# Optimization experiments

Measured on AMD Instinct MI355X. Metric: run time of the kernel, lower is better.

The kernel has to match this reference:

```python
import jax, jax.numpy as jnp
import numpy as np

B, N_HM, K_APP, S = 16, 32, 16, 256

def setup_inputs() -> dict:
    key = jax.random.key(0)
    k1, k2, k3 = jax.random.split(key, 3)
    # x: post-UNet appearance feature map [B, K, S, S]
    x = jax.random.normal(k1, (B, K_APP, S, S), dtype=jnp.float32)
    # raw_tps: raw heatmap logits [B, N, S, S]
    raw_tps = jax.random.normal(k2, (B, N_HM, S, S), dtype=jnp.float32)
    # fitted_cj: non-negative fitted heatmaps [B, N, S, S]
    fitted_cj = jax.random.uniform(k3, (B, N_HM, S, S), dtype=jnp.float32)
    return {"x": x, "raw_tps": raw_tps, "fitted_cj": fitted_cj}

def reference(x, raw_tps, fitted_cj):
    # torch F.softmax on a 2D [S,S] tensor with no dim defaults to dim=1 -> per-row softmax
    p = jax.nn.softmax(raw_tps, axis=-1)                      # [B, N, S, S]
    # attention pooling: app_vec[b,n,k] = sum_{h,w} x[b,k,h,w] * p[b,n,h,w]
    app_vec = jnp.einsum('bkhw,bnhw->bnk', x, p)              # [B, N, K]
    # weighted combine without materializing the [B,N,S,S,K] repeat
    num = jnp.einsum('bnhw,bnk->bhwk', fitted_cj, app_vec)    # [B, S, S, K]
    denom = 1.0 + jnp.sum(fitted_cj, axis=1)[..., None]       # [B, S, S, 1]
    app_enco = num / denom                                     # [B, S, S, K]
    # transpose(2,3) then transpose(1,2): [B,S,S,K] -> [B,K,S,S]
    return jnp.transpose(app_enco, (0, 3, 1, 2))
```

## Files before the change

kernel.cpp:

```cpp
#include <hip/hip_runtime.h>

#define S_DIM 256
#define N_HM 32
#define K_APP 16
#define HG 4

typedef _Float16 half4_t __attribute__((ext_vector_type(4)));
typedef _Float16 half8_t __attribute__((ext_vector_type(8)));
typedef float f32x4 __attribute__((ext_vector_type(4)));

__global__ __launch_bounds__(256, 4) void k1_softmax_pool(
    const float* __restrict__ x,
    const float* __restrict__ raw,
    float* __restrict__ partial)
{
    __shared__ _Float16 p_h[N_HM][264];
    __shared__ _Float16 x_h[K_APP][264];
    __shared__ float    inv_s[N_HM];
    __shared__ float    red[2][64][4];

    const int tid  = threadIdx.x;
    const int wid  = tid >> 6;
    const int lane = tid & 63;
    const int b    = blockIdx.x >> 6;
    const int hg   = blockIdx.x & 63;
    const int h0   = hg * HG;

    const int nh  = wid >> 1;
    const int wq  = wid & 1;
    const int row = lane & 15;
    const int q   = lane >> 4;

    float4 r_raw[8];
    float4 r_x[4];
    f32x4  acc = {0.f, 0.f, 0.f, 0.f};

    {
        const float* rp = raw + (((size_t)(b * N_HM + wid * 8)) << 16) + (h0 << 8) + (lane << 2);
        #pragma unroll
        for (int i = 0; i < 8; ++i) r_raw[i] = *(const float4*)(rp + ((size_t)i << 16));
        const float* xp = x + (((size_t)(b * K_APP + wid * 4)) << 16) + (h0 << 8) + (lane << 2);
        #pragma unroll
        for (int i = 0; i < 4; ++i) r_x[i] = *(const float4*)(xp + ((size_t)i << 16));
    }

    for (int it = 0; it < HG; ++it) {
        #pragma unroll
        for (int i = 0; i < 4; ++i) {
            half4_t hv = { (_Float16)r_x[i].x, (_Float16)r_x[i].y,
                           (_Float16)r_x[i].z, (_Float16)r_x[i].w };
            *(half4_t*)&x_h[wid * 4 + i][lane << 2] = hv;
        }
        #pragma unroll
        for (int i = 0; i < 8; ++i) {
            const int n = wid * 8 + i;
            float e0 = __expf(r_raw[i].x), e1 = __expf(r_raw[i].y);
            float e2 = __expf(r_raw[i].z), e3 = __expf(r_raw[i].w);
            float s = (e0 + e1) + (e2 + e3);
            #pragma unroll
            for (int off = 32; off > 0; off >>= 1) s += __shfl_xor(s, off);
            if (lane == 0) inv_s[n] = 1.0f / s;
            half4_t hv = { (_Float16)e0, (_Float16)e1, (_Float16)e2, (_Float16)e3 };
            *(half4_t*)&p_h[n][lane << 2] = hv;
        }
        __syncthreads();

        if (it + 1 < HG) {
            const int h = h0 + it + 1;
            const float* rp = raw + (((size_t)(b * N_HM + wid * 8)) << 16) + (h << 8) + (lane << 2);
            #pragma unroll
            for (int i = 0; i < 8; ++i) r_raw[i] = *(const float4*)(rp + ((size_t)i << 16));
            const float* xp = x + (((size_t)(b * K_APP + wid * 4)) << 16) + (h << 8) + (lane << 2);
            #pragma unroll
            for (int i = 0; i < 4; ++i) r_x[i] = *(const float4*)(xp + ((size_t)i << 16));
        }

        f32x4 part = {0.f, 0.f, 0.f, 0.f};
        #pragma unroll
        for (int s4 = 0; s4 < 4; ++s4) {
            const int w = wq * 128 + s4 * 32 + q * 8;
            half8_t a = *(const half8_t*)&p_h[nh * 16 + row][w];
            half8_t bb = *(const half8_t*)&x_h[row][w];
            part = __builtin_amdgcn_mfma_f32_16x16x32_f16(a, bb, part, 0, 0, 0);
        }
        const int rb = nh * 16 + q * 4;
        acc.x += part.x * inv_s[rb + 0];
        acc.y += part.y * inv_s[rb + 1];
        acc.z += part.z * inv_s[rb + 2];
        acc.w += part.w * inv_s[rb + 3];
        __syncthreads();
    }

    if (wq == 1) {
        red[nh][lane][0] = acc.x; red[nh][lane][1] = acc.y;
        red[nh][lane][2] = acc.z; red[nh][lane][3] = acc.w;
    }
    __syncthreads();
    if (wq == 0) {
        float* dst = partial + ((size_t)blockIdx.x << 9)
                   + (size_t)(nh * 16 + q * 4) * 16 + row;
        dst[0]  = acc.x + red[nh][lane][0];
        dst[16] = acc.y + red[nh][lane][1];
        dst[32] = acc.z + red[nh][lane][2];
        dst[48] = acc.w + red[nh][lane][3];
    }
}

__global__ __launch_bounds__(256) void k1_reduce(
    const float* __restrict__ partial, float* __restrict__ av)
{
    const int gid = blockIdx.x * 256 + threadIdx.x;
    const int b = gid >> 9;
    const int r = gid & 511;
    const float* p = partial + ((size_t)b << 15) + r;
    float s = 0.0f;
    #pragma unroll 8
    for (int j = 0; j < 64; ++j) s += p[(size_t)j << 9];
    av[gid] = s;
}

__global__ __launch_bounds__(256) void k2_combine(
    const float* __restrict__ fit,
    const float* __restrict__ av,
    float* __restrict__ out)
{
    const int tid = threadIdx.x;
    const int b   = blockIdx.x >> 6;
    const int p4  = ((blockIdx.x & 63) << 8) + tid;

    const float* fb  = fit + (((size_t)(b * N_HM)) << 16) + ((size_t)p4 << 2);
    const float* avb = av + (b << 9);

    float4 num[K_APP];
    #pragma unroll
    for (int k = 0; k < K_APP; ++k) num[k] = make_float4(0.f, 0.f, 0.f, 0.f);
    float4 den = make_float4(1.f, 1.f, 1.f, 1.f);

    #pragma unroll 4
    for (int n = 0; n < N_HM; ++n) {
        float4 f = *(const float4*)(fb + ((size_t)n << 16));
        den.x += f.x; den.y += f.y; den.z += f.z; den.w += f.w;
        const float* a = avb + (n << 4);
        #pragma unroll
        for (int k = 0; k < K_APP; ++k) {
            const float ak = a[k];
            num[k].x += f.x * ak; num[k].y += f.y * ak;
            num[k].z += f.z * ak; num[k].w += f.w * ak;
        }
    }

    const float4 inv = make_float4(1.f / den.x, 1.f / den.y, 1.f / den.z, 1.f / den.w);
    float* ob = out + (((size_t)(b * K_APP)) << 16) + ((size_t)p4 << 2);
    #pragma unroll
    for (int k = 0; k < K_APP; ++k) {
        float4 v = make_float4(num[k].x * inv.x, num[k].y * inv.y,
                               num[k].z * inv.z, num[k].w * inv.w);
        *(float4*)(ob + ((size_t)k << 16)) = v;
    }
}

extern "C" void kernel_launch(void* const* d_in, const int* in_sizes, int n_in,
                              void* d_out, int out_size, void* d_ws, size_t ws_size,
                              hipStream_t stream)
{
    const float* x   = (const float*)d_in[0];
    const float* raw = (const float*)d_in[1];
    const float* fit = (const float*)d_in[2];
    float* out = (float*)d_out;

    float* av      = (float*)d_ws;
    float* partial = (float*)d_ws + 8192;

    k1_softmax_pool<<<16 * (S_DIM / HG), 256, 0, stream>>>(x, raw, partial);
    k1_reduce<<<8192 / 256, 256, 0, stream>>>(partial, av);
    k2_combine<<<16 * 64, 256, 0, stream>>>(fit, av, out);
}
```

Before: 353.1 us.

## Feed MFMA directly from registers, one wave per row and heatmap half

The softmax-pool kernel drops the shared-memory staging, the block barriers and the cross-wave reduction. Each wave now handles one (batch, row, 16-heatmap half): it loads raw and x straight into the MFMA operand layout, computes exp and the row sum in registers, and writes normalized per-row partials. The cost is a partial buffer four times larger and a reduce kernel that sums 256 rows instead of 64. The combine kernel's unroll factor is also raised from 4 to 8.

```diff
diff --git a/kernel.cpp b/kernel.cpp
--- a/kernel.cpp
+++ b/kernel.cpp
@@ -3,107 +3,59 @@
 #define S_DIM 256
 #define N_HM 32
 #define K_APP 16
-#define HG 4
 
-typedef _Float16 half4_t __attribute__((ext_vector_type(4)));
 typedef _Float16 half8_t __attribute__((ext_vector_type(8)));
 typedef float f32x4 __attribute__((ext_vector_type(4)));
 
-__global__ __launch_bounds__(256, 4) void k1_softmax_pool(
+__global__ __launch_bounds__(256) void k1_softmax_pool(
     const float* __restrict__ x,
     const float* __restrict__ raw,
     float* __restrict__ partial)
 {
-    __shared__ _Float16 p_h[N_HM][264];
-    __shared__ _Float16 x_h[K_APP][264];
-    __shared__ float    inv_s[N_HM];
-    __shared__ float    red[2][64][4];
+    const int wid  = threadIdx.x >> 6;
+    const int lane = threadIdx.x & 63;
+    const int gw   = blockIdx.x * 4 + wid;
+    const int pair = gw >> 1;
+    const int nh   = gw & 1;
+    const int b    = pair >> 8;
+    const int h    = pair & 255;
+    const int col  = lane & 15;
+    const int q    = lane >> 4;
 
-    const int tid  = threadIdx.x;
-    const int wid  = tid >> 6;
-    const int lane = tid & 63;
-    const int b    = blockIdx.x >> 6;
-    const int hg   = blockIdx.x & 63;
-    const int h0   = hg * HG;
+    const float* rp = raw + (((size_t)(b * N_HM + nh * 16 + col)) << 16) + (h << 8);
+    const float* xp = x   + (((size_t)(b * K_APP + col)) << 16) + (h << 8);
 
-    const int nh  = wid >> 1;
-    const int wq  = wid & 1;
-    const int row = lane & 15;
-    const int q   = lane >> 4;
+    f32x4 acc = {0.f, 0.f, 0.f, 0.f};
+    float ssum = 0.f;
 
-    float4 r_raw[8];
-    float4 r_x[4];
-    f32x4  acc = {0.f, 0.f, 0.f, 0.f};
+    #pragma unroll
+    for (int c = 0; c < 8; ++c) {
+        const int w0 = c * 32 + q * 8;
+        float4 r0 = *(const float4*)(rp + w0);
+        float4 r1 = *(const float4*)(rp + w0 + 4);
+        float4 x0 = *(const float4*)(xp + w0);
+        float4 x1 = *(const float4*)(xp + w0 + 4);
 
-    {
-        const float* rp = raw + (((size_t)(b * N_HM + wid * 8)) << 16) + (h0 << 8) + (lane << 2);
-        #pragma unroll
-        for (int i = 0; i < 8; ++i) r_raw[i] = *(const float4*)(rp + ((size_t)i << 16));
-        const float* xp = x + (((size_t)(b * K_APP + wid * 4)) << 16) + (h0 << 8) + (lane << 2);
-        #pragma unroll
-        for (int i = 0; i < 4; ++i) r_x[i] = *(const float4*)(xp + ((size_t)i << 16));
+        float e0 = __expf(r0.x), e1 = __expf(r0.y), e2 = __expf(r0.z), e3 = __expf(r0.w);
+        float e4 = __expf(r1.x), e5 = __expf(r1.y), e6 = __expf(r1.z), e7 = __expf(r1.w);
+        ssum += ((e0 + e1) + (e2 + e3)) + ((e4 + e5) + (e6 + e7));
+
+        half8_t a, bb;
+        a[0] = (_Float16)x0.x; a[1] = (_Float16)x0.y; a[2] = (_Float16)x0.z; a[3] = (_Float16)x0.w;
+        a[4] = (_Float16)x1.x; a[5] = (_Float16)x1.y; a[6] = (_Float16)x1.z; a[7] = (_Float16)x1.w;
+        bb[0] = (_Float16)e0;  bb[1] = (_Float16)e1;  bb[2] = (_Float16)e2;  bb[3] = (_Float16)e3;
+        bb[4] = (_Float16)e4;  bb[5] = (_Float16)e5;  bb[6] = (_Float16)e6;  bb[7] = (_Float16)e7;
+
+        acc = __builtin_amdgcn_mfma_f32_16x16x32_f16(a, bb, acc, 0, 0, 0);
     }
 
-    for (int it = 0; it < HG; ++it) {
-        #pragma unroll
-        for (int i = 0; i < 4; ++i) {
-            half4_t hv = { (_Float16)r_x[i].x, (_Float16)r_x[i].y,
-                           (_Float16)r_x[i].z, (_Float16)r_x[i].w };
-            *(half4_t*)&x_h[wid * 4 + i][lane << 2] = hv;
-        }
-        #pragma unroll
-        for (int i = 0; i < 8; ++i) {
-            const int n = wid * 8 + i;
-            float e0 = __expf(r_raw[i].x), e1 = __expf(r_raw[i].y);
-            float e2 = __expf(r_raw[i].z), e3 = __expf(r_raw[i].w);
-            float s = (e0 + e1) + (e2 + e3);
-            #pragma unroll
-            for (int off = 32; off > 0; off >>= 1) s += __shfl_xor(s, off);
-            if (lane == 0) inv_s[n] = 1.0f / s;
-            half4_t hv = { (_Float16)e0, (_Float16)e1, (_Float16)e2, (_Float16)e3 };
-            *(half4_t*)&p_h[n][lane << 2] = hv;
-        }
-        __syncthreads();
+    ssum += __shfl_xor(ssum, 16);
+    ssum += __shfl_xor(ssum, 32);
+    const float inv = 1.0f / ssum;
 
-        if (it + 1 < HG) {
-            const int h = h0 + it + 1;
-            const float* rp = raw + (((size_t)(b * N_HM + wid * 8)) << 16) + (h << 8) + (lane << 2);
-            #pragma unroll
-            for (int i = 0; i < 8; ++i) r_raw[i] = *(const float4*)(rp + ((size_t)i << 16));
-            const float* xp = x + (((size_t)(b * K_APP + wid * 4)) << 16) + (h << 8) + (lane << 2);
-            #pragma unroll
-            for (int i = 0; i < 4; ++i) r_x[i] = *(const float4*)(xp + ((size_t)i << 16));
-        }
-
-        f32x4 part = {0.f, 0.f, 0.f, 0.f};
-        #pragma unroll
-        for (int s4 = 0; s4 < 4; ++s4) {
-            const int w = wq * 128 + s4 * 32 + q * 8;
-            half8_t a = *(const half8_t*)&p_h[nh * 16 + row][w];
-            half8_t bb = *(const half8_t*)&x_h[row][w];
-            part = __builtin_amdgcn_mfma_f32_16x16x32_f16(a, bb, part, 0, 0, 0);
-        }
-        const int rb = nh * 16 + q * 4;
-        acc.x += part.x * inv_s[rb + 0];
-        acc.y += part.y * inv_s[rb + 1];
-        acc.z += part.z * inv_s[rb + 2];
-        acc.w += part.w * inv_s[rb + 3];
-        __syncthreads();
-    }
-
-    if (wq == 1) {
-        red[nh][lane][0] = acc.x; red[nh][lane][1] = acc.y;
-        red[nh][lane][2] = acc.z; red[nh][lane][3] = acc.w;
-    }
-    __syncthreads();
-    if (wq == 0) {
-        float* dst = partial + ((size_t)blockIdx.x << 9)
-                   + (size_t)(nh * 16 + q * 4) * 16 + row;
-        dst[0]  = acc.x + red[nh][lane][0];
-        dst[16] = acc.y + red[nh][lane][1];
-        dst[32] = acc.z + red[nh][lane][2];
-        dst[48] = acc.w + red[nh][lane][3];
-    }
+    float* dst = partial + ((size_t)pair << 9) + ((nh * 16 + col) << 4) + (q << 2);
+    f32x4 v = {acc.x * inv, acc.y * inv, acc.z * inv, acc.w * inv};
+    *(f32x4*)dst = v;
 }
 
 __global__ __launch_bounds__(256) void k1_reduce(
@@ -112,10 +64,10 @@
     const int gid = blockIdx.x * 256 + threadIdx.x;
     const int b = gid >> 9;
     const int r = gid & 511;
-    const float* p = partial + ((size_t)b << 15) + r;
+    const float* p = partial + (((size_t)b) << 17) + r;
     float s = 0.0f;
     #pragma unroll 8
-    for (int j = 0; j < 64; ++j) s += p[(size_t)j << 9];
+    for (int h = 0; h < 256; ++h) s += p[(size_t)h << 9];
     av[gid] = s;
 }
 
@@ -136,7 +88,7 @@
     for (int k = 0; k < K_APP; ++k) num[k] = make_float4(0.f, 0.f, 0.f, 0.f);
     float4 den = make_float4(1.f, 1.f, 1.f, 1.f);
 
-    #pragma unroll 4
+    #pragma unroll 8
     for (int n = 0; n < N_HM; ++n) {
         float4 f = *(const float4*)(fb + ((size_t)n << 16));
         den.x += f.x; den.y += f.y; den.z += f.z; den.w += f.w;
@@ -171,7 +123,7 @@
     float* av      = (float*)d_ws;
     float* partial = (float*)d_ws + 8192;
 
-    k1_softmax_pool<<<16 * (S_DIM / HG), 256, 0, stream>>>(x, raw, partial);
+    k1_softmax_pool<<<2048, 256, 0, stream>>>(x, raw, partial);
     k1_reduce<<<8192 / 256, 256, 0, stream>>>(partial, av);
     k2_combine<<<16 * 64, 256, 0, stream>>>(fit, av, out);
 }
```

Measured after the change: 361.1 us. +2.3%, slower.
